# Kernel tuning notes

Hardware: AMD Instinct MI355X
Metric: run time of the kernel (lower is better)

## Reference

```python
import jax, jax.numpy as jnp
import numpy as np

B, N, V, E, T = 32, 256, 16, 1024, 5
MAX_N, ANNO, ND, VD, A_ACT = 256, 18, 64, 64, 3


def position_encoding_init(n_position, emb_dim):
    pe = np.array([[pos / np.power(10000, 2 * (j // 2) / emb_dim) for j in range(emb_dim)]
                   if pos != 0 else np.zeros(emb_dim) for pos in range(n_position)])
    pe[1:, 0::2] = np.sin(pe[1:, 0::2])
    pe[1:, 1::2] = np.cos(pe[1:, 1::2])
    return jnp.asarray(pe, jnp.float32)


def gru_cell(x, h, Wih, Whh, bih=None, bhh=None):
    # PyTorch GRUCell semantics. Wih: [3H, in], Whh: [3H, H]
    gi = x @ Wih.T + (bih if bih is not None else 0.0)
    gh = h @ Whh.T + (bhh if bhh is not None else 0.0)
    i_r, i_z, i_n = jnp.split(gi, 3, axis=1)
    h_r, h_z, h_n = jnp.split(gh, 3, axis=1)
    r = jax.nn.sigmoid(i_r + h_r)
    z = jax.nn.sigmoid(i_z + h_z)
    n = jnp.tanh(i_n + r * h_n)
    return (1.0 - z) * n + z * h


def setup_inputs() -> dict:
    key = jax.random.key(0)
    ks = jax.random.split(key, 20)
    dec_in = E + ND + 2 * VD
    inp = {
        "annotation": jax.random.normal(ks[0], (B, N, ANNO), jnp.float32),
        "A_out": jax.random.bernoulli(ks[1], 0.05, (B, N, N)).astype(jnp.float32),
        "A_in": jax.random.bernoulli(ks[2], 0.05, (B, N, N)).astype(jnp.float32),
        "from_node": jax.random.randint(ks[3], (B,), 0, MAX_N),
        "vnf_now": jax.random.uniform(ks[4], (B, V), jnp.float32),
        "vnf_all": jax.random.uniform(ks[5], (B, V), jnp.float32),
        "mask": jax.random.randint(ks[6], (B * N,), 0, 2),
        "anno_W": jax.random.normal(ks[7], (ANNO, E), jnp.float32),
        "gru_Wih": jax.random.normal(ks[8], (3 * E, 2 * E), jnp.float32) / np.sqrt(2 * E),
        "gru_Whh": jax.random.normal(ks[9], (3 * E, E), jnp.float32) / np.sqrt(E),
        "vnf_now_W": jax.random.normal(ks[10], (V, VD), jnp.float32),
        "vnf_all_W": jax.random.normal(ks[11], (V, VD), jnp.float32),
        "dgru_Wih": jax.random.normal(ks[12], (6 * E, dec_in), jnp.float32) / np.sqrt(dec_in),
        "dgru_Whh": jax.random.normal(ks[13], (6 * E, 2 * E), jnp.float32) / np.sqrt(2 * E),
        "dgru_bih": jax.random.normal(ks[14], (6 * E,), jnp.float32) * 0.01,
        "dgru_bhh": jax.random.normal(ks[15], (6 * E,), jnp.float32) * 0.01,
        "out_W1": jax.random.normal(ks[16], (E, 2 * E), jnp.float32) / np.sqrt(2 * E),
        "out_b1": jnp.zeros((E,), jnp.float32),
        "out_W2": jax.random.normal(ks[17], (A_ACT, E), jnp.float32) / np.sqrt(E),
        "out_b2": jnp.zeros((A_ACT,), jnp.float32),
        "pos_enc": position_encoding_init(MAX_N, ND),
    }
    return inp


def reference(annotation, A_out, A_in, from_node, vnf_now, vnf_all, mask,
              anno_W, gru_Wih, gru_Whh, vnf_now_W, vnf_all_W,
              dgru_Wih, dgru_Whh, dgru_bih, dgru_bhh,
              out_W1, out_b1, out_W2, out_b2, pos_enc):
    BN = B * N
    # ---- encoder (GG-NN): block-diagonal adjacency matmul == batched matmul ----
    h = annotation.reshape(BN, ANNO) @ anno_W  # [BN, E]

    def step(h, _):
        hb = h.reshape(B, N, E)
        a_out = jnp.einsum('bnm,bme->bne', A_out, hb).reshape(BN, E)
        a_in = jnp.einsum('bnm,bme->bne', A_in, hb).reshape(BN, E)
        a = jnp.concatenate([a_out, a_in], axis=1)  # [BN, 2E]
        return gru_cell(a, h, gru_Wih, gru_Whh), None

    enc_out, _ = jax.lax.scan(step, h, None, length=T)  # [BN, E]

    # ---- decoder step ----
    vn = (vnf_now @ vnf_now_W)[:, None, :]  # [B,1,VD] (repeat over N)
    va = (vnf_all @ vnf_all_W)[:, None, :]
    npos = pos_enc[from_node][:, None, :]   # [B,1,ND]
    vn = jnp.broadcast_to(vn, (B, N, VD)).reshape(BN, VD)
    va = jnp.broadcast_to(va, (B, N, VD)).reshape(BN, VD)
    npos = jnp.broadcast_to(npos, (B, N, ND)).reshape(BN, ND)

    concat_input = jnp.concatenate([enc_out, npos, va, vn], axis=1)
    h0 = jnp.zeros((BN, 2 * E), jnp.float32)
    hidden = gru_cell(concat_input, h0, dgru_Wih, dgru_Whh, dgru_bih, dgru_bhh)

    mid = jax.nn.relu(hidden @ out_W1.T + out_b1)
    output = (mid @ out_W2.T + out_b2).reshape(B, N, A_ACT)

    max_v = jnp.max(output, axis=(1, 2), keepdims=True)  # [B,1,1]
    output = output - (max_v + 1.0)
    mask_f = jnp.where(mask == 1, 1.0, 1e10).astype(jnp.float32).reshape(B, N, 1)
    output = mask_f * output + 1.0

    node_logits = output[:, :, 0]            # [B, N]
    vnf_logits = output[:, :, 1:]            # [B, N, 2]
    return node_logits, vnf_logits, hidden
```

## Files before the change

kernel.cpp:

```cpp
#include <hip/hip_runtime.h>
#include <hip/hip_bf16.h>
#include <math.h>

#define B_ 32
#define N_ 256
#define E_ 1024
#define BN_ 8192

typedef __hip_bfloat16 bf16;
typedef __bf16 bf8v __attribute__((ext_vector_type(8)));
typedef float  f4v  __attribute__((ext_vector_type(4)));

__device__ __forceinline__ float b2f(bf16 v) {
    unsigned short u = *(unsigned short*)&v;
    return __uint_as_float(((unsigned)u) << 16);
}
__device__ __forceinline__ unsigned short f2bu(float f) {
    bf16 h = __float2bfloat16(f);
    return *(unsigned short*)&h;
}
__device__ __forceinline__ float4 load4bf(const bf16* p) {
    ushort4 u = *(const ushort4*)p;
    return make_float4(__uint_as_float((unsigned)u.x << 16),
                       __uint_as_float((unsigned)u.y << 16),
                       __uint_as_float((unsigned)u.z << 16),
                       __uint_as_float((unsigned)u.w << 16));
}
__device__ __forceinline__ void store4bf(bf16* p, float a, float b, float c, float d) {
    ushort4 u = make_ushort4(f2bu(a), f2bu(b), f2bu(c), f2bu(d));
    *(ushort4*)p = u;
}
__device__ __forceinline__ float safe_sigm(float x) {
    x = fminf(fmaxf(x, -40.0f), 40.0f);
    return 1.0f / (1.0f + expf(-x));
}
__device__ __forceinline__ float safe_tanh(float x) {
    x = fminf(fmaxf(x, -15.0f), 15.0f);
    float t = expf(2.0f * x);
    return (t - 1.0f) / (t + 1.0f);
}
__device__ __forceinline__ void glds16(const bf16* g, bf16* l) {
    __builtin_amdgcn_global_load_lds(
        (__attribute__((address_space(1))) const void*)g,
        (__attribute__((address_space(3))) void*)l, 16, 0, 0);
}

__global__ __launch_bounds__(256)
void w2bf_kernel(const float* __restrict__ src, bf16* __restrict__ dst, int n4)
{
    int i = blockIdx.x * 256 + threadIdx.x;
    if (i < n4) {
        float4 v = ((const float4*)src)[i];
        store4bf(dst + (size_t)i * 4, v.x, v.y, v.z, v.w);
    }
}

__global__ __launch_bounds__(256)
void wgpack_kernel(const float* __restrict__ Wih, const float* __restrict__ Whh,
                   bf16* __restrict__ Wg)
{
    const int wr = blockIdx.x;
    const int e16 = wr / 48, rem = wr % 48;
    const int gate = rem >> 4, eL = rem & 15;
    const int e = e16 * 16 + eL;
    const float* s1 = Wih + (size_t)(gate * 1024 + e) * 2048;
    const float* s2 = Whh + (size_t)(gate * 1024 + e) * 1024;
    bf16* d = Wg + (size_t)wr * 3072;
    const int k0 = threadIdx.x * 4;
#pragma unroll
    for (int rep = 0; rep < 2; ++rep) {
        int k = k0 + rep * 1024;
        float4 v = *(const float4*)(s1 + k);
        store4bf(d + k, v.x, v.y, v.z, v.w);
    }
    {
        float4 v = *(const float4*)(s2 + k0);
        store4bf(d + 2048 + k0, v.x, v.y, v.z, v.w);
    }
}

__global__ __launch_bounds__(256)
void anno_kernel(const float* __restrict__ anno, const float* __restrict__ W,
                 float* __restrict__ H)
{
    __shared__ float s[18];
    int row = blockIdx.x;
    if (threadIdx.x < 18) s[threadIdx.x] = anno[row * 18 + threadIdx.x];
    __syncthreads();
    for (int j = threadIdx.x; j < 1024; j += 256) {
        float acc = 0.0f;
#pragma unroll
        for (int k = 0; k < 18; ++k) acc = fmaf(s[k], W[k * 1024 + j], acc);
        H[(size_t)row * 1024 + j] = acc;
    }
}

__global__ __launch_bounds__(256)
void bmm_kernel(const float* __restrict__ Aout, const float* __restrict__ Ain,
                const float* __restrict__ H, bf16* __restrict__ Abuf)
{
    __shared__ float As[16][68];
    __shared__ float Bs[16][68];
    const int z = blockIdx.z;
    const int b = z >> 1, which = z & 1;
    const float* Amat = (which ? Ain : Aout) + (size_t)b * N_ * N_;
    const float* Bmat = H + (size_t)b * N_ * E_;
    const int t = threadIdx.x;
    const int tx = t & 15, ty = t >> 4;
    const int bm = blockIdx.x * 64;
    const int bn = blockIdx.y * 64;
    const int ar = t >> 2, ak = (t & 3) << 2;
    const int kr = t >> 4, kn = (t & 15) << 2;
    float acc[4][4] = {};
    for (int k0 = 0; k0 < N_; k0 += 16) {
        float4 av = *(const float4*)(Amat + (size_t)(bm + ar) * N_ + k0 + ak);
        As[ak + 0][ar] = av.x; As[ak + 1][ar] = av.y;
        As[ak + 2][ar] = av.z; As[ak + 3][ar] = av.w;
        float4 bv = *(const float4*)(Bmat + (size_t)(k0 + kr) * E_ + bn + kn);
        *(float4*)&Bs[kr][kn] = bv;
        __syncthreads();
#pragma unroll
        for (int kk = 0; kk < 16; ++kk) {
            float4 a4 = *(const float4*)&As[kk][ty << 2];
            float4 b4 = *(const float4*)&Bs[kk][tx << 2];
            float am[4] = {a4.x, a4.y, a4.z, a4.w};
            float bb[4] = {b4.x, b4.y, b4.z, b4.w};
#pragma unroll
            for (int i = 0; i < 4; ++i)
#pragma unroll
                for (int j = 0; j < 4; ++j)
                    acc[i][j] = fmaf(am[i], bb[j], acc[i][j]);
        }
        __syncthreads();
    }
#pragma unroll
    for (int i = 0; i < 4; ++i) {
        int row = b * N_ + bm + (ty << 2) + i;
        int col = which * 1024 + bn + (tx << 2);
        store4bf(&Abuf[(size_t)row * 2048 + col], acc[i][0], acc[i][1], acc[i][2], acc[i][3]);
    }
}

__global__ __launch_bounds__(256)
void htrans_kernel(const float* __restrict__ H, bf16* __restrict__ HbT)
{
    __shared__ float s[64][65];
    const int b = blockIdx.z;
    const int e0 = blockIdx.x * 64;
    const int n0 = blockIdx.y * 64;
    const float* Hb = H + (size_t)b * N_ * E_;
    bf16* Tb = HbT + (size_t)b * E_ * N_;
    const int t = threadIdx.x;
    const int tr = t >> 4, tc = (t & 15) << 2;
#pragma unroll
    for (int i = 0; i < 4; ++i) {
        float4 v = *(const float4*)(Hb + (size_t)(n0 + tr + i * 16) * E_ + e0 + tc);
        s[tr + i * 16][tc + 0] = v.x; s[tr + i * 16][tc + 1] = v.y;
        s[tr + i * 16][tc + 2] = v.z; s[tr + i * 16][tc + 3] = v.w;
    }
    __syncthreads();
#pragma unroll
    for (int i = 0; i < 4; ++i) {
        int e = tr + i * 16;
        store4bf(Tb + (size_t)(e0 + e) * N_ + n0 + tc,
                 s[tc + 0][e], s[tc + 1][e], s[tc + 2][e], s[tc + 3][e]);
    }
}

__global__ __launch_bounds__(256)
void bmm_mfma_kernel(const bf16* __restrict__ Aoutb, const bf16* __restrict__ Ainb,
                     const bf16* __restrict__ HbT, bf16* __restrict__ Abuf)
{
    __shared__ bf16 As[64 * 32];
    __shared__ bf16 Bs[64 * 32];
    const int t = threadIdx.x;
    const int lane = t & 63, w = t >> 6;
    const int wm = (w >> 1) * 32, wn = (w & 1) * 32;
    const int z = blockIdx.z, b = z >> 1, which = z & 1;
    const int bm = blockIdx.x * 64, bn = blockIdx.y * 64;
    const int quad = lane >> 4, fr = lane & 15;
    const int srow = t >> 2, slot = t & 3;
    const int g = (slot + ((srow >> 1) & 3)) & 3;
    const int lds_off = srow * 32 + slot * 8;

    f4v acc[2][2];
#pragma unroll
    for (int i = 0; i < 2; ++i)
#pragma unroll
        for (int j = 0; j < 2; ++j) acc[i][j] = (f4v){0.f, 0.f, 0.f, 0.f};

    int aoff[2], boff[2];
#pragma unroll
    for (int i = 0; i < 2; ++i) {
        int arow = wm + 16 * i + fr;
        int s = (quad - ((arow >> 1) & 3)) & 3;
        aoff[i] = arow * 32 + s * 8;
    }
#pragma unroll
    for (int j = 0; j < 2; ++j) {
        int n = wn + 16 * j + fr;
        int s = (quad - ((n >> 1) & 3)) & 3;
        boff[j] = n * 32 + s * 8;
    }

    const bf16* Ap = (which ? Ainb : Aoutb) + (size_t)b * N_ * N_
                   + (size_t)(bm + srow) * N_ + g * 8;
    const bf16* Bp = HbT + (size_t)b * E_ * N_ + (size_t)(bn + srow) * N_ + g * 8;
    for (int k0 = 0; k0 < N_; k0 += 32) {
        float4 av = *(const float4*)(Ap + k0);
        float4 bv4 = *(const float4*)(Bp + k0);
        __syncthreads();
        *(float4*)(As + lds_off) = av;
        *(float4*)(Bs + lds_off) = bv4;
        __syncthreads();
        bf8v af0 = *(const bf8v*)(As + aoff[0]);
        bf8v af1 = *(const bf8v*)(As + aoff[1]);
#pragma unroll
        for (int j = 0; j < 2; ++j) {
            bf8v bv = *(const bf8v*)(Bs + boff[j]);
            acc[0][j] = __builtin_amdgcn_mfma_f32_16x16x32_bf16(af0, bv, acc[0][j], 0, 0, 0);
            acc[1][j] = __builtin_amdgcn_mfma_f32_16x16x32_bf16(af1, bv, acc[1][j], 0, 0, 0);
        }
    }
#pragma unroll
    for (int i = 0; i < 2; ++i)
#pragma unroll
        for (int j = 0; j < 2; ++j)
#pragma unroll
            for (int r = 0; r < 4; ++r) {
                int row = b * N_ + bm + wm + 16 * i + quad * 4 + r;
                int col = which * 1024 + bn + wn + 16 * j + fr;
                Abuf[(size_t)row * 2048 + col] = __float2bfloat16(acc[i][j][r]);
            }
}

__global__ __launch_bounds__(256, 2)
void enc_gru_kernel(const bf16* __restrict__ Aab, const bf16* __restrict__ Wg,
                    const float* __restrict__ Hcur, float* __restrict__ Hnext)
{
    __shared__ __align__(16) bf16 As[128 * 32];
    __shared__ __align__(16) bf16 Bs[192 * 32];
    const int t = threadIdx.x;
    const int lane = t & 63, w = t >> 6;
    const int wm = (w >> 1) * 64;
    const int wnH = (w & 1);
    const int bm = blockIdx.x * 128;
    const int bY = blockIdx.y;
    const int quad = lane >> 4, fr = lane & 15;

    f4v ar[2][4], az[2][4], ani[2][4], anh[2][4];
#pragma unroll
    for (int gq = 0; gq < 2; ++gq)
#pragma unroll
        for (int i = 0; i < 4; ++i) {
            ar[gq][i] = (f4v){0.f, 0.f, 0.f, 0.f};
            az[gq][i] = (f4v){0.f, 0.f, 0.f, 0.f};
            ani[gq][i] = (f4v){0.f, 0.f, 0.f, 0.f};
            anh[gq][i] = (f4v){0.f, 0.f, 0.f, 0.f};
        }

    int aoff[4];
#pragma unroll
    for (int i = 0; i < 4; ++i) {
        int row = wm + 16 * i + fr;
        int s = (quad - ((row >> 1) & 3)) & 3;
        aoff[i] = row * 32 + s * 8;
    }
    int boff[2][3];
#pragma unroll
    for (int gq = 0; gq < 2; ++gq)
#pragma unroll
        for (int gt = 0; gt < 3; ++gt) {
            int nb = wnH * 96 + gq * 48 + gt * 16 + fr;
            int s = (quad - ((nb >> 1) & 3)) & 3;
            boff[gq][gt] = nb * 32 + s * 8;
        }

    const int sr = lane >> 2, ss = lane & 3;
    const int lrA0 = w * 16 + sr;
    const int lrA1 = 64 + w * 16 + sr;
    const int gA0 = (ss + ((lrA0 >> 1) & 3)) & 3;
    const int gA1 = (ss + ((lrA1 >> 1) & 3)) & 3;
    const bf16* apA0 = Aab + (size_t)(bm + lrA0) * 2048 + gA0 * 8;
    const bf16* apA1 = Aab + (size_t)(bm + lrA1) * 2048 + gA1 * 8;
    const int lrB0 = w * 16 + sr, lrB1 = 64 + w * 16 + sr, lrB2 = 128 + w * 16 + sr;
    const int gB0 = (ss + ((lrB0 >> 1) & 3)) & 3;
    const int gB1 = (ss + ((lrB1 >> 1) & 3)) & 3;
    const int gB2 = (ss + ((lrB2 >> 1) & 3)) & 3;
    const bf16* bp0 = Wg + (size_t)(bY * 192 + lrB0) * 3072 + gB0 * 8;
    const bf16* bp1 = Wg + (size_t)(bY * 192 + lrB1) * 3072 + gB1 * 8;
    const bf16* bp2 = Wg + (size_t)(bY * 192 + lrB2) * 3072 + gB2 * 8;
    bf16* ldsA0 = As + (w * 16) * 32;
    bf16* ldsA1 = As + (64 + w * 16) * 32;
    bf16* ldsB0 = Bs + (w * 16) * 32;
    bf16* ldsB1 = Bs + (64 + w * 16) * 32;
    bf16* ldsB2 = Bs + (128 + w * 16) * 32;

    for (int k0 = 0; k0 < 2048; k0 += 32) {
        __syncthreads();
        glds16(apA0 + k0, ldsA0);
        glds16(apA1 + k0, ldsA1);
        glds16(bp0 + k0, ldsB0);
        glds16(bp1 + k0, ldsB1);
        glds16(bp2 + k0, ldsB2);
        __syncthreads();
        bf8v af0 = *(const bf8v*)(As + aoff[0]);
        bf8v af1 = *(const bf8v*)(As + aoff[1]);
        bf8v af2 = *(const bf8v*)(As + aoff[2]);
        bf8v af3 = *(const bf8v*)(As + aoff[3]);
#pragma unroll
        for (int gq = 0; gq < 2; ++gq) {
            bf8v br = *(const bf8v*)(Bs + boff[gq][0]);
            bf8v bz = *(const bf8v*)(Bs + boff[gq][1]);
            bf8v bn = *(const bf8v*)(Bs + boff[gq][2]);
            ar[gq][0] = __builtin_amdgcn_mfma_f32_16x16x32_bf16(af0, br, ar[gq][0], 0, 0, 0);
            ar[gq][1] = __builtin_amdgcn_mfma_f32_16x16x32_bf16(af1, br, ar[gq][1], 0, 0, 0);
            ar[gq][2] = __builtin_amdgcn_mfma_f32_16x16x32_bf16(af2, br, ar[gq][2], 0, 0, 0);
            ar[gq][3] = __builtin_amdgcn_mfma_f32_16x16x32_bf16(af3, br, ar[gq][3], 0, 0, 0);
            az[gq][0] = __builtin_amdgcn_mfma_f32_16x16x32_bf16(af0, bz, az[gq][0], 0, 0, 0);
            az[gq][1] = __builtin_amdgcn_mfma_f32_16x16x32_bf16(af1, bz, az[gq][1], 0, 0, 0);
            az[gq][2] = __builtin_amdgcn_mfma_f32_16x16x32_bf16(af2, bz, az[gq][2], 0, 0, 0);
            az[gq][3] = __builtin_amdgcn_mfma_f32_16x16x32_bf16(af3, bz, az[gq][3], 0, 0, 0);
            ani[gq][0] = __builtin_amdgcn_mfma_f32_16x16x32_bf16(af0, bn, ani[gq][0], 0, 0, 0);
            ani[gq][1] = __builtin_amdgcn_mfma_f32_16x16x32_bf16(af1, bn, ani[gq][1], 0, 0, 0);
            ani[gq][2] = __builtin_amdgcn_mfma_f32_16x16x32_bf16(af2, bn, ani[gq][2], 0, 0, 0);
            ani[gq][3] = __builtin_amdgcn_mfma_f32_16x16x32_bf16(af3, bn, ani[gq][3], 0, 0, 0);
        }
    }

    {
        const int tr = t >> 1;
        const int c0 = (t & 1) * 2;
        const int rr_ = (tr >> 1) & 3;
        const int s0 = (c0 - rr_) & 3;
        const int s1 = (c0 + 1 - rr_) & 3;
        const float* hp = Hcur + (size_t)(bm + tr) * 1024 + c0 * 8;
        for (int k0 = 2048; k0 < 3072; k0 += 32) {
            const int k2 = k0 - 2048;
            float4 f0 = *(const float4*)(hp + k2);
            float4 f1 = *(const float4*)(hp + k2 + 4);
            float4 f2 = *(const float4*)(hp + k2 + 8);
            float4 f3 = *(const float4*)(hp + k2 + 12);
            uint4 u0, u1;
            u0.x = (unsigned)f2bu(f0.x) | ((unsigned)f2bu(f0.y) << 16);
            u0.y = (unsigned)f2bu(f0.z) | ((unsigned)f2bu(f0.w) << 16);
            u0.z = (unsigned)f2bu(f1.x) | ((unsigned)f2bu(f1.y) << 16);
            u0.w = (unsigned)f2bu(f1.z) | ((unsigned)f2bu(f1.w) << 16);
            u1.x = (unsigned)f2bu(f2.x) | ((unsigned)f2bu(f2.y) << 16);
            u1.y = (unsigned)f2bu(f2.z) | ((unsigned)f2bu(f2.w) << 16);
            u1.z = (unsigned)f2bu(f3.x) | ((unsigned)f2bu(f3.y) << 16);
            u1.w = (unsigned)f2bu(f3.z) | ((unsigned)f2bu(f3.w) << 16);
            __syncthreads();
            *(uint4*)(As + tr * 32 + s0 * 8) = u0;
            *(uint4*)(As + tr * 32 + s1 * 8) = u1;
            glds16(bp0 + k0, ldsB0);
            glds16(bp1 + k0, ldsB1);
            glds16(bp2 + k0, ldsB2);
            __syncthreads();
            bf8v af0 = *(const bf8v*)(As + aoff[0]);
            bf8v af1 = *(const bf8v*)(As + aoff[1]);
            bf8v af2 = *(const bf8v*)(As + aoff[2]);
            bf8v af3 = *(const bf8v*)(As + aoff[3]);
#pragma unroll
            for (int gq = 0; gq < 2; ++gq) {
                bf8v br = *(const bf8v*)(Bs + boff[gq][0]);
                bf8v bz = *(const bf8v*)(Bs + boff[gq][1]);
                bf8v bn = *(const bf8v*)(Bs + boff[gq][2]);
                ar[gq][0] = __builtin_amdgcn_mfma_f32_16x16x32_bf16(af0, br, ar[gq][0], 0, 0, 0);
                ar[gq][1] = __builtin_amdgcn_mfma_f32_16x16x32_bf16(af1, br, ar[gq][1], 0, 0, 0);
                ar[gq][2] = __builtin_amdgcn_mfma_f32_16x16x32_bf16(af2, br, ar[gq][2], 0, 0, 0);
                ar[gq][3] = __builtin_amdgcn_mfma_f32_16x16x32_bf16(af3, br, ar[gq][3], 0, 0, 0);
                az[gq][0] = __builtin_amdgcn_mfma_f32_16x16x32_bf16(af0, bz, az[gq][0], 0, 0, 0);
                az[gq][1] = __builtin_amdgcn_mfma_f32_16x16x32_bf16(af1, bz, az[gq][1], 0, 0, 0);
                az[gq][2] = __builtin_amdgcn_mfma_f32_16x16x32_bf16(af2, bz, az[gq][2], 0, 0, 0);
                az[gq][3] = __builtin_amdgcn_mfma_f32_16x16x32_bf16(af3, bz, az[gq][3], 0, 0, 0);
                anh[gq][0] = __builtin_amdgcn_mfma_f32_16x16x32_bf16(af0, bn, anh[gq][0], 0, 0, 0);
                anh[gq][1] = __builtin_amdgcn_mfma_f32_16x16x32_bf16(af1, bn, anh[gq][1], 0, 0, 0);
                anh[gq][2] = __builtin_amdgcn_mfma_f32_16x16x32_bf16(af2, bn, anh[gq][2], 0, 0, 0);
                anh[gq][3] = __builtin_amdgcn_mfma_f32_16x16x32_bf16(af3, bn, anh[gq][3], 0, 0, 0);
            }
        }
    }

#pragma unroll
    for (int gq = 0; gq < 2; ++gq) {
        const int e = bY * 64 + wnH * 32 + gq * 16 + fr;
#pragma unroll
        for (int i = 0; i < 4; ++i) {
#pragma unroll
            for (int r = 0; r < 4; ++r) {
                const int row = bm + wm + 16 * i + quad * 4 + r;
                float hv = Hcur[(size_t)row * 1024 + e];
                float rg = safe_sigm(ar[gq][i][r]);
                float zg = safe_sigm(az[gq][i][r]);
                float ng = safe_tanh(ani[gq][i][r] + rg * anh[gq][i][r]);
                Hnext[(size_t)row * 1024 + e] = (1.0f - zg) * ng + zg * hv;
            }
        }
    }
}

__global__ __launch_bounds__(128)
void vnva_kernel(const float* __restrict__ vnf_now, const float* __restrict__ vnf_all,
                 const float* __restrict__ Wn, const float* __restrict__ Wa,
                 float* __restrict__ vn, float* __restrict__ va)
{
    int b = blockIdx.x, t = threadIdx.x;
    if (t < 64) {
        float s = 0.f;
#pragma unroll
        for (int k = 0; k < 16; ++k) s = fmaf(vnf_now[b * 16 + k], Wn[k * 64 + t], s);
        vn[b * 64 + t] = s;
    } else {
        int d = t - 64;
        float s = 0.f;
#pragma unroll
        for (int k = 0; k < 16; ++k) s = fmaf(vnf_all[b * 16 + k], Wa[k * 64 + d], s);
        va[b * 64 + d] = s;
    }
}

__global__ __launch_bounds__(256)
void concat_kernel(const float* __restrict__ H, const float* __restrict__ pos_enc,
                   const int* __restrict__ from_node, const float* __restrict__ va,
                   const float* __restrict__ vn, bf16* __restrict__ Cc)
{
    int row = blockIdx.x;
    int b = row >> 8;
    int fn = from_node[b];
    bf16* dst = Cc + (size_t)row * 1216;
    for (int c = threadIdx.x; c < 1216; c += 256) {
        float v;
        if (c < 1024)      v = H[(size_t)row * 1024 + c];
        else if (c < 1088) v = pos_enc[fn * 64 + (c - 1024)];
        else if (c < 1152) v = va[b * 64 + (c - 1088)];
        else               v = vn[b * 64 + (c - 1152)];
        dst[c] = __float2bfloat16(v);
    }
}

__global__ __launch_bounds__(256)
void dec_mfma_kernel(const bf16* __restrict__ Cc, const bf16* __restrict__ Wb,
                     const float* __restrict__ bih, const float* __restrict__ bhh,
                     float* __restrict__ hidden)
{
    __shared__ bf16 As[64 * 32];
    __shared__ bf16 Ws[3][64 * 32];
    const int t = threadIdx.x;
    const int lane = t & 63, w = t >> 6;
    const int wm = (w >> 1) * 32, wn = (w & 1) * 32;
    const int bm = blockIdx.x * 64, bn = blockIdx.y * 64;
    const int quad = lane >> 4, fr = lane & 15;
    const int srow = t >> 2, slot = t & 3;
    const int g = (slot + ((srow >> 1) & 3)) & 3;
    const int lds_off = srow * 32 + slot * 8;

    f4v gi[3][2][2];
#pragma unroll
    for (int c = 0; c < 3; ++c)
#pragma unroll
        for (int i = 0; i < 2; ++i)
#pragma unroll
            for (int j = 0; j < 2; ++j) gi[c][i][j] = (f4v){0.f, 0.f, 0.f, 0.f};

    int aoff[2], boff[2];
#pragma unroll
    for (int i = 0; i < 2; ++i) {
        int arow = wm + 16 * i + fr;
        int s = (quad - ((arow >> 1) & 3)) & 3;
        aoff[i] = arow * 32 + s * 8;
    }
#pragma unroll
    for (int j = 0; j < 2; ++j) {
        int n = wn + 16 * j + fr;
        int s = (quad - ((n >> 1) & 3)) & 3;
        boff[j] = n * 32 + s * 8;
    }

    const bf16* Ap = Cc + (size_t)(bm + srow) * 1216 + g * 8;
    const bf16* W0 = Wb + (size_t)(0 * 2048 + bn + srow) * 1216 + g * 8;
    const bf16* W1 = Wb + (size_t)(1 * 2048 + bn + srow) * 1216 + g * 8;
    const bf16* W2 = Wb + (size_t)(2 * 2048 + bn + srow) * 1216 + g * 8;
    for (int k0 = 0; k0 < 1216; k0 += 32) {
        float4 av = *(const float4*)(Ap + k0);
        float4 w0 = *(const float4*)(W0 + k0);
        float4 w1 = *(const float4*)(W1 + k0);
        float4 w2 = *(const float4*)(W2 + k0);
        __syncthreads();
        *(float4*)(As + lds_off) = av;
        *(float4*)(Ws[0] + lds_off) = w0;
        *(float4*)(Ws[1] + lds_off) = w1;
        *(float4*)(Ws[2] + lds_off) = w2;
        __syncthreads();
        bf8v af0 = *(const bf8v*)(As + aoff[0]);
        bf8v af1 = *(const bf8v*)(As + aoff[1]);
#pragma unroll
        for (int c = 0; c < 3; ++c) {
#pragma unroll
            for (int j = 0; j < 2; ++j) {
                bf8v bv = *(const bf8v*)(Ws[c] + boff[j]);
                gi[c][0][j] = __builtin_amdgcn_mfma_f32_16x16x32_bf16(af0, bv, gi[c][0][j], 0, 0, 0);
                gi[c][1][j] = __builtin_amdgcn_mfma_f32_16x16x32_bf16(af1, bv, gi[c][1][j], 0, 0, 0);
            }
        }
    }
#pragma unroll
    for (int j = 0; j < 2; ++j) {
        const int col = bn + wn + 16 * j + fr;
        const float br = bih[col] + bhh[col];
        const float bz = bih[2048 + col] + bhh[2048 + col];
        const float bni = bih[4096 + col];
        const float bnh = bhh[4096 + col];
#pragma unroll
        for (int i = 0; i < 2; ++i) {
#pragma unroll
            for (int r = 0; r < 4; ++r) {
                const int row = bm + wm + 16 * i + quad * 4 + r;
                float rr = safe_sigm(gi[0][i][j][r] + br);
                float zz = safe_sigm(gi[1][i][j][r] + bz);
                float nn = safe_tanh(gi[2][i][j][r] + bni + rr * bnh);
                hidden[(size_t)row * 2048 + col] = (1.0f - zz) * nn;
            }
        }
    }
}

__global__ __launch_bounds__(256)
void out1_mfma_kernel(const float* __restrict__ H, const bf16* __restrict__ W1b,
                      const float* __restrict__ bias, bf16* __restrict__ mid)
{
    __shared__ bf16 As[64 * 32];
    __shared__ bf16 Ws[256 * 32];
    const int t = threadIdx.x;
    const int lane = t & 63, w = t >> 6;
    const int bm = blockIdx.x * 64, bn = blockIdx.y * 256;
    const int quad = lane >> 4, fr = lane & 15;
    const int srow = t >> 2, slot = t & 3;
    const int g = (slot + ((srow >> 1) & 3)) & 3;
    const int lds_off = srow * 32 + slot * 8;

    f4v acc[4][4];
#pragma unroll
    for (int i = 0; i < 4; ++i)
#pragma unroll
        for (int j = 0; j < 4; ++j) acc[i][j] = (f4v){0.f, 0.f, 0.f, 0.f};

    int aoff[4], boff[4];
#pragma unroll
    for (int i = 0; i < 4; ++i) {
        int arow = 16 * i + fr;
        int s = (quad - ((arow >> 1) & 3)) & 3;
        aoff[i] = arow * 32 + s * 8;
    }
#pragma unroll
    for (int j = 0; j < 4; ++j) {
        int n = w * 64 + 16 * j + fr;
        int s = (quad - ((n >> 1) & 3)) & 3;
        boff[j] = n * 32 + s * 8;
    }

    const float* Hp = H + (size_t)(bm + srow) * 2048 + g * 8;
    const bf16* Wp0 = W1b + (size_t)(bn + srow) * 2048 + g * 8;
    const bf16* Wp1 = W1b + (size_t)(bn + srow + 64) * 2048 + g * 8;
    const bf16* Wp2 = W1b + (size_t)(bn + srow + 128) * 2048 + g * 8;
    const bf16* Wp3 = W1b + (size_t)(bn + srow + 192) * 2048 + g * 8;

    for (int k0 = 0; k0 < 2048; k0 += 32) {
        float4 h0 = *(const float4*)(Hp + k0);
        float4 h1 = *(const float4*)(Hp + k0 + 4);
        float4 w0 = *(const float4*)(Wp0 + k0);
        float4 w1 = *(const float4*)(Wp1 + k0);
        float4 w2 = *(const float4*)(Wp2 + k0);
        float4 w3 = *(const float4*)(Wp3 + k0);
        uint4 pk;
        pk.x = (unsigned)f2bu(h0.x) | ((unsigned)f2bu(h0.y) << 16);
        pk.y = (unsigned)f2bu(h0.z) | ((unsigned)f2bu(h0.w) << 16);
        pk.z = (unsigned)f2bu(h1.x) | ((unsigned)f2bu(h1.y) << 16);
        pk.w = (unsigned)f2bu(h1.z) | ((unsigned)f2bu(h1.w) << 16);
        __syncthreads();
        *(uint4*)(As + lds_off) = pk;
        *(float4*)(Ws + lds_off) = w0;
        *(float4*)(Ws + 2048 + lds_off) = w1;
        *(float4*)(Ws + 4096 + lds_off) = w2;
        *(float4*)(Ws + 6144 + lds_off) = w3;
        __syncthreads();
        bf8v af0 = *(const bf8v*)(As + aoff[0]);
        bf8v af1 = *(const bf8v*)(As + aoff[1]);
        bf8v af2 = *(const bf8v*)(As + aoff[2]);
        bf8v af3 = *(const bf8v*)(As + aoff[3]);
#pragma unroll
        for (int j = 0; j < 4; ++j) {
            bf8v bv = *(const bf8v*)(Ws + boff[j]);
            acc[0][j] = __builtin_amdgcn_mfma_f32_16x16x32_bf16(af0, bv, acc[0][j], 0, 0, 0);
            acc[1][j] = __builtin_amdgcn_mfma_f32_16x16x32_bf16(af1, bv, acc[1][j], 0, 0, 0);
            acc[2][j] = __builtin_amdgcn_mfma_f32_16x16x32_bf16(af2, bv, acc[2][j], 0, 0, 0);
            acc[3][j] = __builtin_amdgcn_mfma_f32_16x16x32_bf16(af3, bv, acc[3][j], 0, 0, 0);
        }
    }
#pragma unroll
    for (int j = 0; j < 4; ++j) {
        const int col = bn + w * 64 + 16 * j + fr;
        const float bb = bias[col];
#pragma unroll
        for (int i = 0; i < 4; ++i) {
#pragma unroll
            for (int r = 0; r < 4; ++r) {
                const int row = bm + 16 * i + quad * 4 + r;
                mid[(size_t)row * 1024 + col] = __float2bfloat16(fmaxf(acc[i][j][r] + bb, 0.0f));
            }
        }
    }
}

__global__ __launch_bounds__(64)
void out2_kernel(const bf16* __restrict__ mid, const float* __restrict__ W2,
                 const float* __restrict__ b2, float* __restrict__ outb)
{
    int row = blockIdx.x, t = threadIdx.x;
    float s0 = 0.f, s1 = 0.f, s2 = 0.f;
    for (int k = t; k < 1024; k += 64) {
        float m = b2f(mid[(size_t)row * 1024 + k]);
        s0 = fmaf(m, W2[k], s0);
        s1 = fmaf(m, W2[1024 + k], s1);
        s2 = fmaf(m, W2[2048 + k], s2);
    }
#pragma unroll
    for (int off = 32; off > 0; off >>= 1) {
        s0 += __shfl_down(s0, off, 64);
        s1 += __shfl_down(s1, off, 64);
        s2 += __shfl_down(s2, off, 64);
    }
    if (t == 0) {
        outb[row * 3 + 0] = s0 + b2[0];
        outb[row * 3 + 1] = s1 + b2[1];
        outb[row * 3 + 2] = s2 + b2[2];
    }
}

__global__ __launch_bounds__(64)
void max_kernel(const float* __restrict__ outb, float* __restrict__ maxb)
{
    int b = blockIdx.x, t = threadIdx.x;
    float m = -3.0e38f;
    for (int i = t; i < 768; i += 64) m = fmaxf(m, outb[b * 768 + i]);
#pragma unroll
    for (int off = 32; off > 0; off >>= 1) m = fmaxf(m, __shfl_down(m, off, 64));
    if (t == 0) maxb[b] = m;
}

__global__ __launch_bounds__(256)
void mask_kernel(const float* __restrict__ outb, const float* __restrict__ maxb,
                 const int* __restrict__ mask, float* __restrict__ out)
{
    int idx = blockIdx.x * 256 + threadIdx.x;
    if (idx >= BN_ * 3) return;
    int row = idx / 3, c = idx - row * 3;
    int b = row >> 8;
    float v = outb[idx] - (maxb[b] + 1.0f);
    float mf = (mask[row] == 1) ? 1.0f : 1e10f;
    v = mf * v + 1.0f;
    if (c == 0) out[row] = v;
    else        out[8192 + row * 2 + (c - 1)] = v;
}

extern "C" void kernel_launch(void* const* d_in, const int* in_sizes, int n_in,
                              void* d_out, int out_size, void* d_ws, size_t ws_size,
                              hipStream_t stream)
{
    const float* annotation = (const float*)d_in[0];
    const float* A_out      = (const float*)d_in[1];
    const float* A_in       = (const float*)d_in[2];
    const int*   from_node  = (const int*)d_in[3];
    const float* vnf_now    = (const float*)d_in[4];
    const float* vnf_all    = (const float*)d_in[5];
    const int*   mask       = (const int*)d_in[6];
    const float* anno_W     = (const float*)d_in[7];
    const float* gru_Wih    = (const float*)d_in[8];
    const float* gru_Whh    = (const float*)d_in[9];
    const float* vnf_now_W  = (const float*)d_in[10];
    const float* vnf_all_W  = (const float*)d_in[11];
    const float* dgru_Wih   = (const float*)d_in[12];
    const float* dgru_bih   = (const float*)d_in[14];
    const float* dgru_bhh   = (const float*)d_in[15];
    const float* out_W1     = (const float*)d_in[16];
    const float* out_b1     = (const float*)d_in[17];
    const float* out_W2     = (const float*)d_in[18];
    const float* out_b2     = (const float*)d_in[19];
    const float* pos_enc    = (const float*)d_in[20];
    float* out = (float*)d_out;

    bf16*  Abuf = (bf16*)d_ws;
    bf16*  Wenc = Abuf + (size_t)8192 * 2048;
    bf16*  Wg   = Wenc;
    bf16*  WihbD = Wenc;
    bf16*  W1b  = Wenc;
    float* fbuf = (float*)(Wenc + (size_t)9437184);
    float* vnb  = fbuf;
    float* vab  = vnb + 2048;
    float* outb = vab + 2048;
    float* maxb = outb + 24576;
    bf16*  Aoutb = (bf16*)(maxb + 32);
    bf16*  Ainb  = Aoutb + (size_t)32 * 256 * 256;
    bf16*  HbT   = Ainb + (size_t)32 * 256 * 256;

    const size_t NEED_FULL = (size_t)(16777216 + 9437184) * 2 + 28704 * 4
                           + (size_t)(4194304 + 8388608) * 2;
    const bool full = ws_size >= NEED_FULL;

    float* hidden = out + 24576;
    float* H0 = hidden;
    float* H1 = H0 + (size_t)8192 * 1024;
    bf16* Cc  = Abuf;
    bf16* mid = Abuf;

    wgpack_kernel<<<3072, 256, 0, stream>>>(gru_Wih, gru_Whh, Wg);
    if (full) {
        w2bf_kernel<<<2048, 256, 0, stream>>>(A_out, Aoutb, 32 * 256 * 256 / 4);
        w2bf_kernel<<<2048, 256, 0, stream>>>(A_in,  Ainb,  32 * 256 * 256 / 4);
    }

    anno_kernel<<<8192, 256, 0, stream>>>(annotation, anno_W, H0);

    const float* hc = H0;
    float* hn = H1;
    for (int s = 0; s < 5; ++s) {
        if (full) {
            htrans_kernel<<<dim3(16, 4, 32), 256, 0, stream>>>(hc, HbT);
            bmm_mfma_kernel<<<dim3(4, 16, 64), 256, 0, stream>>>(Aoutb, Ainb, HbT, Abuf);
        } else {
            bmm_kernel<<<dim3(4, 16, 64), 256, 0, stream>>>(A_out, A_in, hc, Abuf);
        }
        enc_gru_kernel<<<dim3(64, 16), 256, 0, stream>>>(Abuf, Wg, hc, hn);
        float* tmp = (float*)hc; hc = hn; hn = tmp;
    }

    vnva_kernel<<<32, 128, 0, stream>>>(vnf_now, vnf_all, vnf_now_W, vnf_all_W, vnb, vab);
    concat_kernel<<<8192, 256, 0, stream>>>(hc, pos_enc, from_node, vab, vnb, Cc);

    w2bf_kernel<<<7296, 256, 0, stream>>>(dgru_Wih, WihbD, 6144 * 1216 / 4);
    dec_mfma_kernel<<<dim3(128, 32), 256, 0, stream>>>(Cc, WihbD, dgru_bih, dgru_bhh, hidden);

    w2bf_kernel<<<2048, 256, 0, stream>>>(out_W1, W1b, 1024 * 2048 / 4);
    out1_mfma_kernel<<<dim3(128, 4), 256, 0, stream>>>(hidden, W1b, out_b1, mid);

    out2_kernel<<<8192, 64, 0, stream>>>(mid, out_W2, out_b2, outb);
    max_kernel<<<32, 64, 0, stream>>>(outb, maxb);
    mask_kernel<<<96, 256, 0, stream>>>(outb, maxb, mask, out);
}
```

Measured before the change: 1.647 ms.

## Double-buffer encoder GRU LDS loads and retile decoder GRU with gate-packed weights

The encoder GRU's first GEMM phase now uses two LDS buffers and prefetches the next K-slice with direct global-to-LDS loads while MFMAs run on the current slice. This halves the barriers per iteration and overlaps load latency with compute. The decoder GRU input GEMM is replaced by a new kernel that copies the encoder's 128x192 tile, double-buffered and gate-interleaved, fed by a new packing kernel that reorders the weights by gate. In exchange, LDS use per block doubles, which may limit occupancy, and the packed layout must match the new tile mapping.

```diff
diff --git a/kernel.cpp b/kernel.cpp
--- a/kernel.cpp
+++ b/kernel.cpp
@@ -44,6 +44,8 @@
         (__attribute__((address_space(1))) const void*)g,
         (__attribute__((address_space(3))) void*)l, 16, 0, 0);
 }
+
+#define MFMA16(d, a, b) d = __builtin_amdgcn_mfma_f32_16x16x32_bf16(a, b, d, 0, 0, 0)
 
 __global__ __launch_bounds__(256)
 void w2bf_kernel(const float* __restrict__ src, bf16* __restrict__ dst, int n4)
@@ -76,6 +78,21 @@
     {
         float4 v = *(const float4*)(s2 + k0);
         store4bf(d + 2048 + k0, v.x, v.y, v.z, v.w);
+    }
+}
+
+__global__ __launch_bounds__(256)
+void dgpack_kernel(const float* __restrict__ Wih, bf16* __restrict__ Wg)
+{
+    const int wr = blockIdx.x;
+    const int e16 = wr / 48, rem = wr % 48;
+    const int gate = rem >> 4, eL = rem & 15;
+    const int e = e16 * 16 + eL;
+    const float* s = Wih + (size_t)(gate * 2048 + e) * 1216;
+    bf16* d = Wg + (size_t)wr * 1216;
+    for (int k4 = threadIdx.x; k4 < 304; k4 += 256) {
+        float4 v = *(const float4*)(s + k4 * 4);
+        store4bf(d + k4 * 4, v.x, v.y, v.z, v.w);
     }
 }
 
@@ -218,8 +235,8 @@
 #pragma unroll
         for (int j = 0; j < 2; ++j) {
             bf8v bv = *(const bf8v*)(Bs + boff[j]);
-            acc[0][j] = __builtin_amdgcn_mfma_f32_16x16x32_bf16(af0, bv, acc[0][j], 0, 0, 0);
-            acc[1][j] = __builtin_amdgcn_mfma_f32_16x16x32_bf16(af1, bv, acc[1][j], 0, 0, 0);
+            MFMA16(acc[0][j], af0, bv);
+            MFMA16(acc[1][j], af1, bv);
         }
     }
 #pragma unroll
@@ -238,8 +255,8 @@
 void enc_gru_kernel(const bf16* __restrict__ Aab, const bf16* __restrict__ Wg,
                     const float* __restrict__ Hcur, float* __restrict__ Hnext)
 {
-    __shared__ __align__(16) bf16 As[128 * 32];
-    __shared__ __align__(16) bf16 Bs[192 * 32];
+    __shared__ __align__(16) bf16 As[2 * 128 * 32];
+    __shared__ __align__(16) bf16 Bs[2 * 192 * 32];
     const int t = threadIdx.x;
     const int lane = t & 63, w = t >> 6;
     const int wm = (w >> 1) * 64;
@@ -290,42 +307,49 @@
     const bf16* bp0 = Wg + (size_t)(bY * 192 + lrB0) * 3072 + gB0 * 8;
     const bf16* bp1 = Wg + (size_t)(bY * 192 + lrB1) * 3072 + gB1 * 8;
     const bf16* bp2 = Wg + (size_t)(bY * 192 + lrB2) * 3072 + gB2 * 8;
-    bf16* ldsA0 = As + (w * 16) * 32;
-    bf16* ldsA1 = As + (64 + w * 16) * 32;
-    bf16* ldsB0 = Bs + (w * 16) * 32;
-    bf16* ldsB1 = Bs + (64 + w * 16) * 32;
-    bf16* ldsB2 = Bs + (128 + w * 16) * 32;
-
+    const int oA0 = (w * 16) * 32, oA1 = (64 + w * 16) * 32;
+    const int oB0 = (w * 16) * 32, oB1 = (64 + w * 16) * 32, oB2 = (128 + w * 16) * 32;
+
+#define ENC_STEP(Ab, Bb, AN) do {                                              \
+    bf8v af0 = *(const bf8v*)((Ab) + aoff[0]);                                 \
+    bf8v af1 = *(const bf8v*)((Ab) + aoff[1]);                                 \
+    bf8v af2 = *(const bf8v*)((Ab) + aoff[2]);                                 \
+    bf8v af3 = *(const bf8v*)((Ab) + aoff[3]);                                 \
+    _Pragma("unroll")                                                          \
+    for (int gq = 0; gq < 2; ++gq) {                                           \
+        bf8v br_ = *(const bf8v*)((Bb) + boff[gq][0]);                         \
+        bf8v bz_ = *(const bf8v*)((Bb) + boff[gq][1]);                         \
+        bf8v bn_ = *(const bf8v*)((Bb) + boff[gq][2]);                         \
+        MFMA16(ar[gq][0], af0, br_); MFMA16(ar[gq][1], af1, br_);              \
+        MFMA16(ar[gq][2], af2, br_); MFMA16(ar[gq][3], af3, br_);              \
+        MFMA16(az[gq][0], af0, bz_); MFMA16(az[gq][1], af1, bz_);              \
+        MFMA16(az[gq][2], af2, bz_); MFMA16(az[gq][3], af3, bz_);              \
+        MFMA16(AN[gq][0], af0, bn_); MFMA16(AN[gq][1], af1, bn_);              \
+        MFMA16(AN[gq][2], af2, bn_); MFMA16(AN[gq][3], af3, bn_);              \
+    }                                                                          \
+} while (0)
+
+    glds16(apA0, As + oA0);
+    glds16(apA1, As + oA1);
+    glds16(bp0, Bs + oB0);
+    glds16(bp1, Bs + oB1);
+    glds16(bp2, Bs + oB2);
+    __syncthreads();
+    int cur = 0;
     for (int k0 = 0; k0 < 2048; k0 += 32) {
+        const int nb = cur ^ 1;
+        if (k0 + 32 < 2048) {
+            glds16(apA0 + k0 + 32, As + nb * 4096 + oA0);
+            glds16(apA1 + k0 + 32, As + nb * 4096 + oA1);
+            glds16(bp0 + k0 + 32, Bs + nb * 6144 + oB0);
+            glds16(bp1 + k0 + 32, Bs + nb * 6144 + oB1);
+            glds16(bp2 + k0 + 32, Bs + nb * 6144 + oB2);
+        }
+        const bf16* Ab = As + cur * 4096;
+        const bf16* Bb = Bs + cur * 6144;
+        ENC_STEP(Ab, Bb, ani);
         __syncthreads();
-        glds16(apA0 + k0, ldsA0);
-        glds16(apA1 + k0, ldsA1);
-        glds16(bp0 + k0, ldsB0);
-        glds16(bp1 + k0, ldsB1);
-        glds16(bp2 + k0, ldsB2);
-        __syncthreads();
-        bf8v af0 = *(const bf8v*)(As + aoff[0]);
-        bf8v af1 = *(const bf8v*)(As + aoff[1]);
-        bf8v af2 = *(const bf8v*)(As + aoff[2]);
-        bf8v af3 = *(const bf8v*)(As + aoff[3]);
-#pragma unroll
-        for (int gq = 0; gq < 2; ++gq) {
-            bf8v br = *(const bf8v*)(Bs + boff[gq][0]);
-            bf8v bz = *(const bf8v*)(Bs + boff[gq][1]);
-            bf8v bn = *(const bf8v*)(Bs + boff[gq][2]);
-            ar[gq][0] = __builtin_amdgcn_mfma_f32_16x16x32_bf16(af0, br, ar[gq][0], 0, 0, 0);
-            ar[gq][1] = __builtin_amdgcn_mfma_f32_16x16x32_bf16(af1, br, ar[gq][1], 0, 0, 0);
-            ar[gq][2] = __builtin_amdgcn_mfma_f32_16x16x32_bf16(af2, br, ar[gq][2], 0, 0, 0);
-            ar[gq][3] = __builtin_amdgcn_mfma_f32_16x16x32_bf16(af3, br, ar[gq][3], 0, 0, 0);
-            az[gq][0] = __builtin_amdgcn_mfma_f32_16x16x32_bf16(af0, bz, az[gq][0], 0, 0, 0);
-            az[gq][1] = __builtin_amdgcn_mfma_f32_16x16x32_bf16(af1, bz, az[gq][1], 0, 0, 0);
-            az[gq][2] = __builtin_amdgcn_mfma_f32_16x16x32_bf16(af2, bz, az[gq][2], 0, 0, 0);
-            az[gq][3] = __builtin_amdgcn_mfma_f32_16x16x32_bf16(af3, bz, az[gq][3], 0, 0, 0);
-            ani[gq][0] = __builtin_amdgcn_mfma_f32_16x16x32_bf16(af0, bn, ani[gq][0], 0, 0, 0);
-            ani[gq][1] = __builtin_amdgcn_mfma_f32_16x16x32_bf16(af1, bn, ani[gq][1], 0, 0, 0);
-            ani[gq][2] = __builtin_amdgcn_mfma_f32_16x16x32_bf16(af2, bn, ani[gq][2], 0, 0, 0);
-            ani[gq][3] = __builtin_amdgcn_mfma_f32_16x16x32_bf16(af3, bn, ani[gq][3], 0, 0, 0);
-        }
+        cur = nb;
     }
 
     {
@@ -353,32 +377,11 @@
             __syncthreads();
             *(uint4*)(As + tr * 32 + s0 * 8) = u0;
             *(uint4*)(As + tr * 32 + s1 * 8) = u1;
-            glds16(bp0 + k0, ldsB0);
-            glds16(bp1 + k0, ldsB1);
-            glds16(bp2 + k0, ldsB2);
+            glds16(bp0 + k0, Bs + oB0);
+            glds16(bp1 + k0, Bs + oB1);
+            glds16(bp2 + k0, Bs + oB2);
             __syncthreads();
-            bf8v af0 = *(const bf8v*)(As + aoff[0]);
-            bf8v af1 = *(const bf8v*)(As + aoff[1]);
-            bf8v af2 = *(const bf8v*)(As + aoff[2]);
-            bf8v af3 = *(const bf8v*)(As + aoff[3]);
-#pragma unroll
-            for (int gq = 0; gq < 2; ++gq) {
-                bf8v br = *(const bf8v*)(Bs + boff[gq][0]);
-                bf8v bz = *(const bf8v*)(Bs + boff[gq][1]);
-                bf8v bn = *(const bf8v*)(Bs + boff[gq][2]);
-                ar[gq][0] = __builtin_amdgcn_mfma_f32_16x16x32_bf16(af0, br, ar[gq][0], 0, 0, 0);
-                ar[gq][1] = __builtin_amdgcn_mfma_f32_16x16x32_bf16(af1, br, ar[gq][1], 0, 0, 0);
-                ar[gq][2] = __builtin_amdgcn_mfma_f32_16x16x32_bf16(af2, br, ar[gq][2], 0, 0, 0);
-                ar[gq][3] = __builtin_amdgcn_mfma_f32_16x16x32_bf16(af3, br, ar[gq][3], 0, 0, 0);
-                az[gq][0] = __builtin_amdgcn_mfma_f32_16x16x32_bf16(af0, bz, az[gq][0], 0, 0, 0);
-                az[gq][1] = __builtin_amdgcn_mfma_f32_16x16x32_bf16(af1, bz, az[gq][1], 0, 0, 0);
-                az[gq][2] = __builtin_amdgcn_mfma_f32_16x16x32_bf16(af2, bz, az[gq][2], 0, 0, 0);
-                az[gq][3] = __builtin_amdgcn_mfma_f32_16x16x32_bf16(af3, bz, az[gq][3], 0, 0, 0);
-                anh[gq][0] = __builtin_amdgcn_mfma_f32_16x16x32_bf16(af0, bn, anh[gq][0], 0, 0, 0);
-                anh[gq][1] = __builtin_amdgcn_mfma_f32_16x16x32_bf16(af1, bn, anh[gq][1], 0, 0, 0);
-                anh[gq][2] = __builtin_amdgcn_mfma_f32_16x16x32_bf16(af2, bn, anh[gq][2], 0, 0, 0);
-                anh[gq][3] = __builtin_amdgcn_mfma_f32_16x16x32_bf16(af3, bn, anh[gq][3], 0, 0, 0);
-            }
+            ENC_STEP(As, Bs, anh);
         }
     }
 
@@ -395,6 +398,123 @@
                 float zg = safe_sigm(az[gq][i][r]);
                 float ng = safe_tanh(ani[gq][i][r] + rg * anh[gq][i][r]);
                 Hnext[(size_t)row * 1024 + e] = (1.0f - zg) * ng + zg * hv;
+            }
+        }
+    }
+#undef ENC_STEP
+}
+
+__global__ __launch_bounds__(256, 2)
+void dec_gru_kernel(const bf16* __restrict__ Cc, const bf16* __restrict__ Wg,
+                    const float* __restrict__ bih, const float* __restrict__ bhh,
+                    float* __restrict__ hidden)
+{
+    __shared__ __align__(16) bf16 As[2 * 128 * 32];
+    __shared__ __align__(16) bf16 Bs[2 * 192 * 32];
+    const int t = threadIdx.x;
+    const int lane = t & 63, w = t >> 6;
+    const int wm = (w >> 1) * 64;
+    const int wnH = (w & 1);
+    const int bm = blockIdx.x * 128;
+    const int bY = blockIdx.y;
+    const int quad = lane >> 4, fr = lane & 15;
+
+    f4v ag[3][2][4];
+#pragma unroll
+    for (int c = 0; c < 3; ++c)
+#pragma unroll
+        for (int gq = 0; gq < 2; ++gq)
+#pragma unroll
+            for (int i = 0; i < 4; ++i) ag[c][gq][i] = (f4v){0.f, 0.f, 0.f, 0.f};
+
+    int aoff[4];
+#pragma unroll
+    for (int i = 0; i < 4; ++i) {
+        int row = wm + 16 * i + fr;
+        int s = (quad - ((row >> 1) & 3)) & 3;
+        aoff[i] = row * 32 + s * 8;
+    }
+    int boff[2][3];
+#pragma unroll
+    for (int gq = 0; gq < 2; ++gq)
+#pragma unroll
+        for (int gt = 0; gt < 3; ++gt) {
+            int nb = wnH * 96 + gq * 48 + gt * 16 + fr;
+            int s = (quad - ((nb >> 1) & 3)) & 3;
+            boff[gq][gt] = nb * 32 + s * 8;
+        }
+
+    const int sr = lane >> 2, ss = lane & 3;
+    const int lrA0 = w * 16 + sr;
+    const int lrA1 = 64 + w * 16 + sr;
+    const int gA0 = (ss + ((lrA0 >> 1) & 3)) & 3;
+    const int gA1 = (ss + ((lrA1 >> 1) & 3)) & 3;
+    const bf16* apA0 = Cc + (size_t)(bm + lrA0) * 1216 + gA0 * 8;
+    const bf16* apA1 = Cc + (size_t)(bm + lrA1) * 1216 + gA1 * 8;
+    const int lrB0 = w * 16 + sr, lrB1 = 64 + w * 16 + sr, lrB2 = 128 + w * 16 + sr;
+    const int gB0 = (ss + ((lrB0 >> 1) & 3)) & 3;
+    const int gB1 = (ss + ((lrB1 >> 1) & 3)) & 3;
+    const int gB2 = (ss + ((lrB2 >> 1) & 3)) & 3;
+    const bf16* bp0 = Wg + (size_t)(bY * 192 + lrB0) * 1216 + gB0 * 8;
+    const bf16* bp1 = Wg + (size_t)(bY * 192 + lrB1) * 1216 + gB1 * 8;
+    const bf16* bp2 = Wg + (size_t)(bY * 192 + lrB2) * 1216 + gB2 * 8;
+    const int oA0 = (w * 16) * 32, oA1 = (64 + w * 16) * 32;
+    const int oB0 = (w * 16) * 32, oB1 = (64 + w * 16) * 32, oB2 = (128 + w * 16) * 32;
+
+    glds16(apA0, As + oA0);
+    glds16(apA1, As + oA1);
+    glds16(bp0, Bs + oB0);
+    glds16(bp1, Bs + oB1);
+    glds16(bp2, Bs + oB2);
+    __syncthreads();
+    int cur = 0;
+    for (int k0 = 0; k0 < 1216; k0 += 32) {
+        const int nb = cur ^ 1;
+        if (k0 + 32 < 1216) {
+            glds16(apA0 + k0 + 32, As + nb * 4096 + oA0);
+            glds16(apA1 + k0 + 32, As + nb * 4096 + oA1);
+            glds16(bp0 + k0 + 32, Bs + nb * 6144 + oB0);
+            glds16(bp1 + k0 + 32, Bs + nb * 6144 + oB1);
+            glds16(bp2 + k0 + 32, Bs + nb * 6144 + oB2);
+        }
+        const bf16* Ab = As + cur * 4096;
+        const bf16* Bb = Bs + cur * 6144;
+        bf8v af0 = *(const bf8v*)(Ab + aoff[0]);
+        bf8v af1 = *(const bf8v*)(Ab + aoff[1]);
+        bf8v af2 = *(const bf8v*)(Ab + aoff[2]);
+        bf8v af3 = *(const bf8v*)(Ab + aoff[3]);
+#pragma unroll
+        for (int gq = 0; gq < 2; ++gq) {
+            bf8v br_ = *(const bf8v*)(Bb + boff[gq][0]);
+            bf8v bz_ = *(const bf8v*)(Bb + boff[gq][1]);
+            bf8v bn_ = *(const bf8v*)(Bb + boff[gq][2]);
+            MFMA16(ag[0][gq][0], af0, br_); MFMA16(ag[0][gq][1], af1, br_);
+            MFMA16(ag[0][gq][2], af2, br_); MFMA16(ag[0][gq][3], af3, br_);
+            MFMA16(ag[1][gq][0], af0, bz_); MFMA16(ag[1][gq][1], af1, bz_);
+            MFMA16(ag[1][gq][2], af2, bz_); MFMA16(ag[1][gq][3], af3, bz_);
+            MFMA16(ag[2][gq][0], af0, bn_); MFMA16(ag[2][gq][1], af1, bn_);
+            MFMA16(ag[2][gq][2], af2, bn_); MFMA16(ag[2][gq][3], af3, bn_);
+        }
+        __syncthreads();
+        cur = nb;
+    }
+
+#pragma unroll
+    for (int gq = 0; gq < 2; ++gq) {
+        const int e = bY * 64 + wnH * 32 + gq * 16 + fr;
+        const float br = bih[e] + bhh[e];
+        const float bz = bih[2048 + e] + bhh[2048 + e];
+        const float bni = bih[4096 + e];
+        const float bnh = bhh[4096 + e];
+#pragma unroll
+        for (int i = 0; i < 4; ++i) {
+#pragma unroll
+            for (int r = 0; r < 4; ++r) {
+                const int row = bm + wm + 16 * i + quad * 4 + r;
+                float rr = safe_sigm(ag[0][gq][i][r] + br);
+                float zz = safe_sigm(ag[1][gq][i][r] + bz);
+                float nn = safe_tanh(ag[2][gq][i][r] + bni + rr * bnh);
+                hidden[(size_t)row * 2048 + e] = (1.0f - zz) * nn;
             }
         }
     }
@@ -436,92 +556,6 @@
         else if (c < 1152) v = va[b * 64 + (c - 1088)];
         else               v = vn[b * 64 + (c - 1152)];
         dst[c] = __float2bfloat16(v);
-    }
-}
-
-__global__ __launch_bounds__(256)
-void dec_mfma_kernel(const bf16* __restrict__ Cc, const bf16* __restrict__ Wb,
-                     const float* __restrict__ bih, const float* __restrict__ bhh,
-                     float* __restrict__ hidden)
-{
-    __shared__ bf16 As[64 * 32];
-    __shared__ bf16 Ws[3][64 * 32];
-    const int t = threadIdx.x;
-    const int lane = t & 63, w = t >> 6;
-    const int wm = (w >> 1) * 32, wn = (w & 1) * 32;
-    const int bm = blockIdx.x * 64, bn = blockIdx.y * 64;
-    const int quad = lane >> 4, fr = lane & 15;
-    const int srow = t >> 2, slot = t & 3;
-    const int g = (slot + ((srow >> 1) & 3)) & 3;
-    const int lds_off = srow * 32 + slot * 8;
-
-    f4v gi[3][2][2];
-#pragma unroll
-    for (int c = 0; c < 3; ++c)
-#pragma unroll
-        for (int i = 0; i < 2; ++i)
-#pragma unroll
-            for (int j = 0; j < 2; ++j) gi[c][i][j] = (f4v){0.f, 0.f, 0.f, 0.f};
-
-    int aoff[2], boff[2];
-#pragma unroll
-    for (int i = 0; i < 2; ++i) {
-        int arow = wm + 16 * i + fr;
-        int s = (quad - ((arow >> 1) & 3)) & 3;
-        aoff[i] = arow * 32 + s * 8;
-    }
-#pragma unroll
-    for (int j = 0; j < 2; ++j) {
-        int n = wn + 16 * j + fr;
-        int s = (quad - ((n >> 1) & 3)) & 3;
-        boff[j] = n * 32 + s * 8;
-    }
-
-    const bf16* Ap = Cc + (size_t)(bm + srow) * 1216 + g * 8;
-    const bf16* W0 = Wb + (size_t)(0 * 2048 + bn + srow) * 1216 + g * 8;
-    const bf16* W1 = Wb + (size_t)(1 * 2048 + bn + srow) * 1216 + g * 8;
-    const bf16* W2 = Wb + (size_t)(2 * 2048 + bn + srow) * 1216 + g * 8;
-    for (int k0 = 0; k0 < 1216; k0 += 32) {
-        float4 av = *(const float4*)(Ap + k0);
-        float4 w0 = *(const float4*)(W0 + k0);
-        float4 w1 = *(const float4*)(W1 + k0);
-        float4 w2 = *(const float4*)(W2 + k0);
-        __syncthreads();
-        *(float4*)(As + lds_off) = av;
-        *(float4*)(Ws[0] + lds_off) = w0;
-        *(float4*)(Ws[1] + lds_off) = w1;
-        *(float4*)(Ws[2] + lds_off) = w2;
-        __syncthreads();
-        bf8v af0 = *(const bf8v*)(As + aoff[0]);
-        bf8v af1 = *(const bf8v*)(As + aoff[1]);
-#pragma unroll
-        for (int c = 0; c < 3; ++c) {
-#pragma unroll
-            for (int j = 0; j < 2; ++j) {
-                bf8v bv = *(const bf8v*)(Ws[c] + boff[j]);
-                gi[c][0][j] = __builtin_amdgcn_mfma_f32_16x16x32_bf16(af0, bv, gi[c][0][j], 0, 0, 0);
-                gi[c][1][j] = __builtin_amdgcn_mfma_f32_16x16x32_bf16(af1, bv, gi[c][1][j], 0, 0, 0);
-            }
-        }
-    }
-#pragma unroll
-    for (int j = 0; j < 2; ++j) {
-        const int col = bn + wn + 16 * j + fr;
-        const float br = bih[col] + bhh[col];
-        const float bz = bih[2048 + col] + bhh[2048 + col];
-        const float bni = bih[4096 + col];
-        const float bnh = bhh[4096 + col];
-#pragma unroll
-        for (int i = 0; i < 2; ++i) {
-#pragma unroll
-            for (int r = 0; r < 4; ++r) {
-                const int row = bm + wm + 16 * i + quad * 4 + r;
-                float rr = safe_sigm(gi[0][i][j][r] + br);
-                float zz = safe_sigm(gi[1][i][j][r] + bz);
-                float nn = safe_tanh(gi[2][i][j][r] + bni + rr * bnh);
-                hidden[(size_t)row * 2048 + col] = (1.0f - zz) * nn;
-            }
-        }
     }
 }
 
@@ -591,10 +625,10 @@
 #pragma unroll
         for (int j = 0; j < 4; ++j) {
             bf8v bv = *(const bf8v*)(Ws + boff[j]);
-            acc[0][j] = __builtin_amdgcn_mfma_f32_16x16x32_bf16(af0, bv, acc[0][j], 0, 0, 0);
-            acc[1][j] = __builtin_amdgcn_mfma_f32_16x16x32_bf16(af1, bv, acc[1][j], 0, 0, 0);
-            acc[2][j] = __builtin_amdgcn_mfma_f32_16x16x32_bf16(af2, bv, acc[2][j], 0, 0, 0);
-            acc[3][j] = __builtin_amdgcn_mfma_f32_16x16x32_bf16(af3, bv, acc[3][j], 0, 0, 0);
+            MFMA16(acc[0][j], af0, bv);
+            MFMA16(acc[1][j], af1, bv);
+            MFMA16(acc[2][j], af2, bv);
+            MFMA16(acc[3][j], af3, bv);
         }
     }
 #pragma unroll
@@ -692,7 +726,7 @@
     bf16*  Abuf = (bf16*)d_ws;
     bf16*  Wenc = Abuf + (size_t)8192 * 2048;
     bf16*  Wg   = Wenc;
-    bf16*  WihbD = Wenc;
+    bf16*  WgD  = Wenc;
     bf16*  W1b  = Wenc;
     float* fbuf = (float*)(Wenc + (size_t)9437184);
     float* vnb  = fbuf;
@@ -737,8 +771,8 @@
     vnva_kernel<<<32, 128, 0, stream>>>(vnf_now, vnf_all, vnf_now_W, vnf_all_W, vnb, vab);
     concat_kernel<<<8192, 256, 0, stream>>>(hc, pos_enc, from_node, vab, vnb, Cc);
 
-    w2bf_kernel<<<7296, 256, 0, stream>>>(dgru_Wih, WihbD, 6144 * 1216 / 4);
-    dec_mfma_kernel<<<dim3(128, 32), 256, 0, stream>>>(Cc, WihbD, dgru_bih, dgru_bhh, hidden);
+    dgpack_kernel<<<6144, 256, 0, stream>>>(dgru_Wih, WgD);
+    dec_gru_kernel<<<dim3(64, 32), 256, 0, stream>>>(Cc, WgD, dgru_bih, dgru_bhh, hidden);
 
     w2bf_kernel<<<2048, 256, 0, stream>>>(out_W1, W1b, 1024 * 2048 / 4);
     out1_mfma_kernel<<<dim3(128, 4), 256, 0, stream>>>(hidden, W1b, out_b1, mid);
```

After: 1.668 ms. About the same (+1.3%).
